# Kernel tuning notes

Measured on AMD Instinct MI355X. Metric: run time of the kernel, lower is better.

The kernel has to match this reference:

```python
import jax, jax.numpy as jnp
import numpy as np

B, NQ, NK = 4, 1024, 1536
DQ = DK = DV = 1024
DI = 4096
H = 16
EPS = 1e-5

def _ln(x, g, b):
    mu = jnp.mean(x, axis=-1, keepdims=True)
    var = jnp.mean((x - mu) ** 2, axis=-1, keepdims=True)
    return (x - mu) * jax.lax.rsqrt(var + EPS) * g + b

def setup_inputs() -> dict:
    key = jax.random.key(0)
    ks = jax.random.split(key, 20)
    s = 0.02
    inp = {
        "Q": jax.random.normal(ks[0], (B, NQ, DQ), jnp.float32),
        "K": jax.random.normal(ks[1], (B, NK, DK), jnp.float32),
        "knn_masks": jax.random.normal(ks[2], (B * H, NQ, 1024), jnp.float32),
        "mask_pos": 1024,
        "Wq": jax.random.normal(ks[3], (DQ, DV), jnp.float32) * s,
        "bq": jnp.zeros((DV,), jnp.float32),
        "Wk": jax.random.normal(ks[4], (DK, DV), jnp.float32) * s,
        "bk": jnp.zeros((DV,), jnp.float32),
        "Wv": jax.random.normal(ks[5], (DK, DV), jnp.float32) * s,
        "bv": jnp.zeros((DV,), jnp.float32),
        "Wo0": jax.random.normal(ks[6], (DV, DV), jnp.float32) * s,
        "bo0": jnp.zeros((DV,), jnp.float32),
        "Wo": jax.random.normal(ks[7], (DV, DI), jnp.float32) * s,
        "bo": jnp.zeros((DI,), jnp.float32),
        "Wo2": jax.random.normal(ks[8], (DI, DV), jnp.float32) * s,
        "bo2": jnp.zeros((DV,), jnp.float32),
        "g0": jnp.ones((DV,), jnp.float32),
        "beta0": jnp.zeros((DV,), jnp.float32),
        "g1": jnp.ones((DV,), jnp.float32),
        "beta1": jnp.zeros((DV,), jnp.float32),
    }
    return inp

def reference(Q, K, knn_masks, mask_pos, Wq, bq, Wk, bk, Wv, bv,
              Wo0, bo0, Wo, bo, Wo2, bo2, g0, beta0, g1, beta1):
    dh = DV // H
    q = Q @ Wq + bq                      # [B,NQ,DV]
    k = K @ Wk + bk                      # [B,NK,DV]
    v = K @ Wv + bv
    # torch cat(split(.,dh,2),0) -> head-major [H,B,N,dh]
    qh = q.reshape(B, NQ, H, dh).transpose(2, 0, 1, 3)
    kh = k[:, :mask_pos].reshape(B, mask_pos, H, dh).transpose(2, 0, 1, 3)
    vh = v[:, :mask_pos].reshape(B, mask_pos, H, dh).transpose(2, 0, 1, 3)
    logits = jnp.einsum("hbqd,hbkd->hbqk", qh, kh) / jnp.sqrt(jnp.float32(DV))
    logits = logits + knn_masks.reshape(H, B, NQ, mask_pos)
    attn = jax.nn.softmax(logits, axis=-1)
    o = jnp.einsum("hbqk,hbkd->hbqd", attn, vh)   # [H,B,NQ,dh]
    o = o.transpose(1, 2, 0, 3).reshape(B, NQ, DV)  # concat heads
    o = o @ Wo0 + bo0
    O = q + o
    O = _ln(O, g0, beta0)
    ff = jax.nn.relu(O @ Wo + bo) @ Wo2 + bo2
    O = O + ff
    O = _ln(O, g1, beta1)
    return O
```

## Files before the change

### kernel.cpp

```cpp
#include <hip/hip_runtime.h>
#include <hip/hip_bf16.h>

typedef unsigned short u16;
typedef __attribute__((ext_vector_type(4))) short bf16x4;
typedef __attribute__((ext_vector_type(8))) short bf16x8;
typedef __attribute__((ext_vector_type(4))) float f32x4;

static __device__ __forceinline__ u16 f2b(float f){
  union { float f; unsigned u; } v; v.f = f;
  unsigned r = v.u + 0x7fffu + ((v.u >> 16) & 1u);
  return (u16)(r >> 16);
}
static __device__ __forceinline__ float b2f(u16 h){
  union { unsigned u; float f; } v; v.u = ((unsigned)h) << 16; return v.f;
}
static __device__ __forceinline__ void gld_lds16(const void* g, void* l){
  __builtin_amdgcn_global_load_lds((const __attribute__((address_space(1))) void*)g,
                                   (__attribute__((address_space(3))) void*)l, 16, 0, 0);
}

__global__ __launch_bounds__(256) void cvt_qk(const float* __restrict__ Q,
                                              const float* __restrict__ K,
                                              u16* __restrict__ Qb,
                                              u16* __restrict__ Kb){
  const int row = blockIdx.x, t = threadIdx.x;
  const float* src; u16* dst;
  if (row < 4096){
    src = Q + (size_t)row * 1024; dst = Qb + (size_t)row * 1024;
  } else {
    int r = row - 4096;
    size_t ir = (size_t)r + (size_t)(r >> 10) * 512;
    src = K + ir * 1024; dst = Kb + (size_t)r * 1024;
  }
  const float4 v = *(const float4*)(src + t * 4);
  bf16x4 o;
  o[0] = (short)f2b(v.x); o[1] = (short)f2b(v.y);
  o[2] = (short)f2b(v.z); o[3] = (short)f2b(v.w);
  *(bf16x4*)(dst + t * 4) = o;
}

static __device__ __forceinline__ void transpose_body(const float* __restrict__ in,
                                                      u16* __restrict__ out, int K, int N){
  __shared__ float tile[64][65];
  const int k0 = blockIdx.y * 64, n0 = blockIdx.x * 64;
  const int t = threadIdx.x, tr = t >> 4, tc = t & 15;
#pragma unroll
  for (int i = 0; i < 4; i++){
    int r = tr + i * 16;
    float4 v = *(const float4*)(in + (size_t)(k0 + r) * N + n0 + tc * 4);
    tile[r][tc*4+0] = v.x; tile[r][tc*4+1] = v.y; tile[r][tc*4+2] = v.z; tile[r][tc*4+3] = v.w;
  }
  __syncthreads();
#pragma unroll
  for (int i = 0; i < 4; i++){
    int nr = tr + i * 16;
    bf16x4 pk;
#pragma unroll
    for (int j = 0; j < 4; j++) pk[j] = (short)f2b(tile[tc*4+j][nr]);
    *(bf16x4*)(out + (size_t)(n0 + nr) * K + k0 + tc * 4) = pk;
  }
}

__global__ __launch_bounds__(256) void transpose_cvt_k(const float* __restrict__ in,
                                                       u16* __restrict__ out, int K, int N){
  transpose_body(in, out, K, N);
}

__global__ __launch_bounds__(256) void transpose_cvt4(const float* __restrict__ i0, u16* __restrict__ o0,
                                                      const float* __restrict__ i1, u16* __restrict__ o1,
                                                      const float* __restrict__ i2, u16* __restrict__ o2,
                                                      const float* __restrict__ i3, u16* __restrict__ o3){
  const float* in; u16* out;
  switch (blockIdx.z){
    case 0: in = i0; out = o0; break;
    case 1: in = i1; out = o1; break;
    case 2: in = i2; out = o2; break;
    default: in = i3; out = o3; break;
  }
  transpose_body(in, out, 1024, 1024);
}

static __device__ __forceinline__ void gemm_mainloop(const u16* __restrict__ A,
                                                     const u16* __restrict__ Bt,
                                                     int lda, int ldb, int kbeg, int kend,
                                                     int m0, int n0,
                                                     u16* lA, u16* lB, f32x4 acc[4][4]){
  const int t = threadIdx.x, w = t >> 6, l = t & 63;
  const int wr = w >> 1, wc = w & 1;
  const int lrow = l >> 3, lc8 = l & 7;
  const int c = l & 15, g = l >> 4;
  for (int k0 = kbeg; k0 < kend; k0 += 64){
#pragma unroll
    for (int i = 0; i < 4; i++){
      int ch = w * 4 + i;
      int r  = ch * 8 + lrow;
      gld_lds16(A  + (size_t)(m0 + r) * lda + k0 + lc8 * 8, lA + ch * 512);
      gld_lds16(Bt + (size_t)(n0 + r) * ldb + k0 + lc8 * 8, lB + ch * 512);
    }
    __syncthreads();
#pragma unroll
    for (int ks = 0; ks < 2; ks++){
      bf16x8 af[4], bfr[4];
#pragma unroll
      for (int mi = 0; mi < 4; mi++){
        int row = wr * 64 + mi * 16 + c;
        af[mi] = *(const bf16x8*)((const char*)lA + row * 128 + ks * 64 + g * 16);
      }
#pragma unroll
      for (int ni = 0; ni < 4; ni++){
        int row = wc * 64 + ni * 16 + c;
        bfr[ni] = *(const bf16x8*)((const char*)lB + row * 128 + ks * 64 + g * 16);
      }
#pragma unroll
      for (int mi = 0; mi < 4; mi++)
#pragma unroll
        for (int ni = 0; ni < 4; ni++)
          acc[mi][ni] = __builtin_amdgcn_mfma_f32_16x16x32_bf16(af[mi], bfr[ni], acc[mi][ni], 0, 0, 0);
    }
    __syncthreads();
  }
}

__global__ __launch_bounds__(256) void gemm_sk2(const u16* __restrict__ A,
                                                const u16* __restrict__ Bt,
                                                float* __restrict__ pout){
  __shared__ u16 lA[128 * 64];
  __shared__ u16 lB[128 * 64];
  const int t = threadIdx.x, w = t >> 6, l = t & 63;
  const int m0 = blockIdx.y * 128, n0 = blockIdx.x * 128;
  const int wr = w >> 1, wc = w & 1;
  const int c = l & 15, g = l >> 4;
  const int kbeg = blockIdx.z * 512;

  f32x4 acc[4][4];
#pragma unroll
  for (int i = 0; i < 4; i++)
#pragma unroll
    for (int j = 0; j < 4; j++) acc[i][j] = (f32x4){0.f, 0.f, 0.f, 0.f};

  gemm_mainloop(A, Bt, 1024, 1024, kbeg, kbeg + 512, m0, n0, lA, lB, acc);

  float* po = pout + ((size_t)blockIdx.z << 22);
#pragma unroll
  for (int ni = 0; ni < 4; ni++){
    int n = n0 + wc * 64 + ni * 16 + c;
#pragma unroll
    for (int mi = 0; mi < 4; mi++){
      int row0 = m0 + wr * 64 + mi * 16 + 4 * g;
#pragma unroll
      for (int r = 0; r < 4; r++)
        po[(size_t)(row0 + r) * 1024 + n] = acc[mi][ni][r];
    }
  }
}

static __device__ __forceinline__ void loop8p(const u16* __restrict__ A,
                                              const u16* __restrict__ Bt,
                                              int lda, int ldb, int kbeg, int NT,
                                              int m0, int n0,
                                              u16 (*sA)[2][8192], u16 (*sB)[2][8192],
                                              f32x4 acc[8][4]){
  const int t = threadIdx.x, w = t >> 6, l = t & 63;
  const int wr = w >> 2, wc = w & 3;
  const int c = l & 15, g = l >> 4;
  const int sr = t >> 3, scb = (t & 7) << 4;

  auto stA = [&](int d, int h, int T){
#pragma unroll
    for (int i = 0; i < 2; i++){
      int row = i * 64 + sr;
      int Lb  = scb ^ ((row & 7) << 4);
      gld_lds16(A + (size_t)(m0 + h * 128 + row) * lda + kbeg + T * 64 + (Lb >> 1),
                (char*)&sA[d][h][0] + i * 8192 + t * 16);
    }
  };
  auto stB = [&](int d, int h, int T){
#pragma unroll
    for (int i = 0; i < 2; i++){
      int row = i * 64 + sr;
      int Lb  = scb ^ ((row & 7) << 4);
      gld_lds16(Bt + (size_t)(n0 + h * 128 + row) * ldb + kbeg + T * 64 + (Lb >> 1),
                (char*)&sB[d][h][0] + i * 8192 + t * 16);
    }
  };

  stB(0, 0, 0); stB(0, 1, 0); stA(0, 0, 0); stA(0, 1, 0);
  stB(1, 0, 1); stB(1, 1, 1);

  bf16x8 bfr[4][2];
  for (int T = 0; T < NT; ++T){
    const int d = T & 1;
    const char* pa = (const char*)&sA[d][wr][0];
    const char* pb = (const char*)&sB[d][wc >> 1][0];
#pragma unroll
    for (int q = 0; q < 4; ++q){
      if (q == 0){
        if (T + 1 < NT) asm volatile("s_waitcnt vmcnt(4)" ::: "memory");
        else            asm volatile("s_waitcnt vmcnt(0)" ::: "memory");
        asm volatile("" ::: "memory");
        __builtin_amdgcn_s_barrier();
        asm volatile("" ::: "memory");
#pragma unroll
        for (int nf = 0; nf < 4; ++nf){
          int lr = (wc & 1) * 64 + nf * 16 + c;
#pragma unroll
          for (int ks = 0; ks < 2; ++ks)
            bfr[nf][ks] = *(const bf16x8*)(pb + lr * 128 + ((ks * 64 + g * 16) ^ ((lr & 7) << 4)));
        }
      }
      bf16x8 af[2][2];
#pragma unroll
      for (int mi = 0; mi < 2; ++mi){
        int lr = (q * 2 + mi) * 16 + c;
#pragma unroll
        for (int ks = 0; ks < 2; ++ks)
          af[mi][ks] = *(const bf16x8*)(pa + lr * 128 + ((ks * 64 + g * 16) ^ ((lr & 7) << 4)));
      }
      if      (q == 0){ if (T + 1 < NT) stA(d ^ 1, 0, T + 1); }
      else if (q == 1){ if (T + 1 < NT) stA(d ^ 1, 1, T + 1); }
      else if (q == 2){ if (T + 2 < NT) stB(d, 0, T + 2); }
      else            { if (T + 2 < NT) stB(d, 1, T + 2); }
      __builtin_amdgcn_s_setprio(1);
#pragma unroll
      for (int mi = 0; mi < 2; ++mi)
#pragma unroll
        for (int nf = 0; nf < 4; ++nf)
#pragma unroll
          for (int ks = 0; ks < 2; ++ks)
            acc[q * 2 + mi][nf] =
              __builtin_amdgcn_mfma_f32_16x16x32_bf16(af[mi][ks], bfr[nf][ks], acc[q * 2 + mi][nf], 0, 0, 0);
      __builtin_amdgcn_s_setprio(0);
      asm volatile("" ::: "memory");
      __builtin_amdgcn_s_barrier();
      asm volatile("" ::: "memory");
    }
  }
}

template<int EPI>
__global__ __launch_bounds__(512, 2) void gemm8p(const u16* __restrict__ A,
                                                 const u16* __restrict__ Bt,
                                                 const float* __restrict__ bias,
                                                 void* __restrict__ outp,
                                                 int lda, int ldb, int ldout,
                                                 int ksz, int NT){
  __shared__ u16 sA[2][2][8192];
  __shared__ u16 sB[2][2][8192];
  const int t = threadIdx.x, w = t >> 6, l = t & 63;
  const int wr = w >> 2, wc = w & 3;
  const int c = l & 15, g = l >> 4;
  const int m0 = blockIdx.y * 256, n0 = blockIdx.x * 256;

  f32x4 acc[8][4];
#pragma unroll
  for (int i = 0; i < 8; i++)
#pragma unroll
    for (int j = 0; j < 4; j++) acc[i][j] = (f32x4){0.f, 0.f, 0.f, 0.f};

  loop8p(A, Bt, lda, ldb, blockIdx.z * ksz, NT, m0, n0, sA, sB, acc);

  if (EPI == 0){
    u16* out = (u16*)outp;
#pragma unroll
    for (int nf = 0; nf < 4; ++nf){
      int n = n0 + wc * 64 + nf * 16 + c;
      float bv = bias[n];
#pragma unroll
      for (int mf = 0; mf < 8; ++mf){
        int row0 = m0 + wr * 128 + mf * 16 + 4 * g;
#pragma unroll
        for (int r = 0; r < 4; ++r)
          out[(size_t)(row0 + r) * ldout + n] = f2b(fmaxf(acc[mf][nf][r] + bv, 0.f));
      }
    }
  } else {
    float* po = (float*)outp + ((size_t)blockIdx.z << 22);
#pragma unroll
    for (int nf = 0; nf < 4; ++nf){
      int n = n0 + wc * 64 + nf * 16 + c;
#pragma unroll
      for (int mf = 0; mf < 8; ++mf){
        int row0 = m0 + wr * 128 + mf * 16 + 4 * g;
#pragma unroll
        for (int r = 0; r < 4; ++r)
          po[(size_t)(row0 + r) * 1024 + n] = acc[mf][nf][r];
      }
    }
  }
}

__global__ __launch_bounds__(512, 2) void gemm8p_qkv(const u16* __restrict__ Qb,
                                                     const u16* __restrict__ Kb,
                                                     const u16* __restrict__ Wq_t,
                                                     const u16* __restrict__ Wk_t,
                                                     const u16* __restrict__ Wv_t,
                                                     const float* __restrict__ bq,
                                                     const float* __restrict__ bk,
                                                     const float* __restrict__ bv,
                                                     u16* __restrict__ qb,
                                                     u16* __restrict__ kbf,
                                                     u16* __restrict__ vtb){
  __shared__ u16 sA[2][2][8192];
  __shared__ u16 sB[2][2][8192];
  const int bx = blockIdx.x, sel = bx >> 2;
  const u16* A    = sel ? Kb : Qb;
  const u16* Bt   = (sel == 0) ? Wq_t : (sel == 1) ? Wk_t : Wv_t;
  const float* bi = (sel == 0) ? bq   : (sel == 1) ? bk   : bv;
  const int t = threadIdx.x, w = t >> 6, l = t & 63;
  const int wr = w >> 2, wc = w & 3;
  const int c = l & 15, g = l >> 4;
  const int m0 = blockIdx.y * 256, n0 = (bx & 3) * 256;

  f32x4 acc[8][4];
#pragma unroll
  for (int i = 0; i < 8; i++)
#pragma unroll
    for (int j = 0; j < 4; j++) acc[i][j] = (f32x4){0.f, 0.f, 0.f, 0.f};

  loop8p(A, Bt, 1024, 1024, 0, 16, m0, n0, sA, sB, acc);

#pragma unroll
  for (int nf = 0; nf < 4; ++nf){
    int n = n0 + wc * 64 + nf * 16 + c;
    float bv_ = bi[n];
#pragma unroll
    for (int mf = 0; mf < 8; ++mf){
      int row0 = m0 + wr * 128 + mf * 16 + 4 * g;
      if (sel == 2){
        bf16x4 pk;
#pragma unroll
        for (int r = 0; r < 4; ++r) pk[r] = (short)f2b(acc[mf][nf][r] + bv_);
        int bb = row0 >> 10, key = row0 & 1023;
        *(bf16x4*)(vtb + ((size_t)bb << 20) + (size_t)n * 1024 + key) = pk;
      } else {
        u16* out = sel ? kbf : qb;
#pragma unroll
        for (int r = 0; r < 4; ++r)
          out[(size_t)(row0 + r) * 1024 + n] = f2b(acc[mf][nf][r] + bv_);
      }
    }
  }
}

__global__ __launch_bounds__(256) void comb_ln0(const float* __restrict__ pp,
                                                const float* __restrict__ bias,
                                                const u16* __restrict__ res,
                                                const float* __restrict__ gw,
                                                const float* __restrict__ bw,
                                                u16* __restrict__ out){
  const int row = blockIdx.x, t = threadIdx.x, w = t >> 6, l = t & 63;
  const size_t i4 = (size_t)row * 1024 + t * 4;
  f32x4 a = *(const f32x4*)(pp + i4);
  f32x4 b = *(const f32x4*)(pp + (1ull << 22) + i4);
  bf16x4 rv = *(const bf16x4*)(res + i4);
  float xs[4], s = 0.f, sq = 0.f;
#pragma unroll
  for (int j = 0; j < 4; j++){
    xs[j] = a[j] + b[j] + bias[t * 4 + j] + b2f((u16)rv[j]);
    s += xs[j]; sq += xs[j] * xs[j];
  }
#pragma unroll
  for (int o = 32; o; o >>= 1){ s += __shfl_xor(s, o); sq += __shfl_xor(sq, o); }
  __shared__ float rs[4], rq[4];
  if (l == 0){ rs[w] = s; rq[w] = sq; }
  __syncthreads();
  s  = rs[0] + rs[1] + rs[2] + rs[3];
  sq = rq[0] + rq[1] + rq[2] + rq[3];
  const float mu   = s * (1.f / 1024.f);
  const float var  = sq * (1.f / 1024.f) - mu * mu;
  const float rstd = rsqrtf(var + 1e-5f);
  bf16x4 o;
#pragma unroll
  for (int j = 0; j < 4; j++) o[j] = (short)f2b((xs[j]-mu)*rstd*gw[t*4+j] + bw[t*4+j]);
  *(bf16x4*)(out + i4) = o;
}

__global__ __launch_bounds__(256) void comb_ln1(const float* __restrict__ pp,
                                                const float* __restrict__ bias,
                                                const u16* __restrict__ res,
                                                const float* __restrict__ gw,
                                                const float* __restrict__ bw,
                                                float* __restrict__ out){
  const int row = blockIdx.x, t = threadIdx.x, w = t >> 6, l = t & 63;
  const size_t i4 = (size_t)row * 1024 + t * 4;
  f32x4 a = *(const f32x4*)(pp + i4);
#pragma unroll
  for (int z = 1; z < 4; z++){
    f32x4 p = *(const f32x4*)(pp + ((size_t)z << 22) + i4);
    a[0] += p[0]; a[1] += p[1]; a[2] += p[2]; a[3] += p[3];
  }
  bf16x4 rv = *(const bf16x4*)(res + i4);
  float xs[4], s = 0.f, sq = 0.f;
#pragma unroll
  for (int j = 0; j < 4; j++){
    xs[j] = a[j] + bias[t * 4 + j] + b2f((u16)rv[j]);
    s += xs[j]; sq += xs[j] * xs[j];
  }
#pragma unroll
  for (int o = 32; o; o >>= 1){ s += __shfl_xor(s, o); sq += __shfl_xor(sq, o); }
  __shared__ float rs[4], rq[4];
  if (l == 0){ rs[w] = s; rq[w] = sq; }
  __syncthreads();
  s  = rs[0] + rs[1] + rs[2] + rs[3];
  sq = rq[0] + rq[1] + rq[2] + rq[3];
  const float mu   = s * (1.f / 1024.f);
  const float var  = sq * (1.f / 1024.f) - mu * mu;
  const float rstd = rsqrtf(var + 1e-5f);
  float4 o4;
  o4.x = (xs[0]-mu)*rstd*gw[t*4+0] + bw[t*4+0];
  o4.y = (xs[1]-mu)*rstd*gw[t*4+1] + bw[t*4+1];
  o4.z = (xs[2]-mu)*rstd*gw[t*4+2] + bw[t*4+2];
  o4.w = (xs[3]-mu)*rstd*gw[t*4+3] + bw[t*4+3];
  *((float4*)out + (size_t)row * 256 + t) = o4;
}

__global__ __launch_bounds__(256, 4) void attn_k(const u16* __restrict__ qb,
                                                 const u16* __restrict__ kb,
                                                 const u16* __restrict__ vt,
                                                 const float* __restrict__ mask,
                                                 u16* __restrict__ ob){
  __shared__ u16 sK[2][4096];
  __shared__ u16 sV[2][4096];

  const int t = threadIdx.x, w = t >> 6, l = t & 63;
  const int c = l & 15, g = l >> 4;
  const int q0 = blockIdx.x * 64, h = blockIdx.y, b = blockIdx.z;
  const int qrow = q0 + w * 16 + c;
  const size_t qoff = ((size_t)(b * 1024 + qrow)) * 1024 + h * 64;
  const bf16x8 bq0 = *(const bf16x8*)(qb + qoff + g * 8);
  const bf16x8 bq1 = *(const bf16x8*)(qb + qoff + 32 + g * 8);
  const u16* kbase = kb + ((size_t)b * 1024) * 1024 + h * 64;
  const u16* vbase = vt + ((size_t)b << 20) + (size_t)(h * 64) * 1024;
  const float* mbase = mask + ((size_t)(h * 4 + b) * 1024 + qrow) * 1024;

  const int lr3 = l >> 3, lc3 = l & 7;
  const int ch0 = w * 2;

  auto stage = [&](int buf, int kv){
#pragma unroll
    for (int i = 0; i < 2; i++){
      int ch  = ch0 + i;
      int row = ch * 8 + lr3;
      int L   = (lc3 * 16) ^ ((row & 7) << 4);
      gld_lds16(kbase + (size_t)(kv + row) * 1024 + (L >> 1), &sK[buf][ch * 512]);
      gld_lds16(vbase + (size_t)row * 1024 + kv + (L >> 1),   &sV[buf][ch * 512]);
    }
  };

  float m = -INFINITY, lsum = 0.f;
  f32x4 acc[4];
#pragma unroll
  for (int f = 0; f < 4; f++) acc[f] = (f32x4){0.f, 0.f, 0.f, 0.f};

  stage(0, 0);
  asm volatile("" ::: "memory");
  f32x4 mc[4], mn[4];
#pragma unroll
  for (int nf = 0; nf < 4; nf++) mc[nf] = *(const f32x4*)(mbase + nf * 16 + g * 4);

  const int sw = (c & 7) << 4;
  int cur = 0;
  for (int it = 0; it < 16; ++it){
    const int kv = it * 64;
    asm volatile("s_waitcnt vmcnt(4)" ::: "memory");
    __builtin_amdgcn_s_barrier();
    asm volatile("" ::: "memory");

    if (it < 15){
      stage(cur ^ 1, kv + 64);
      asm volatile("" ::: "memory");
#pragma unroll
      for (int nf = 0; nf < 4; nf++)
        mn[nf] = *(const f32x4*)(mbase + kv + 64 + nf * 16 + g * 4);
    }

    const char* kt = (const char*)sK[cur];
    f32x4 st[4];
#pragma unroll
    for (int nf = 0; nf < 4; nf++){
      const char* kr = kt + (nf * 16 + c) * 128;
      bf16x8 ak0 = *(const bf16x8*)(kr + ((g * 16) ^ sw));
      bf16x8 ak1 = *(const bf16x8*)(kr + ((64 + g * 16) ^ sw));
      f32x4 z = (f32x4){0.f, 0.f, 0.f, 0.f};
      z = __builtin_amdgcn_mfma_f32_16x16x32_bf16(ak0, bq0, z, 0, 0, 0);
      z = __builtin_amdgcn_mfma_f32_16x16x32_bf16(ak1, bq1, z, 0, 0, 0);
      st[nf] = z;
    }

    float tmax = -INFINITY;
#pragma unroll
    for (int nf = 0; nf < 4; nf++)
#pragma unroll
      for (int r = 0; r < 4; r++){
        float v = st[nf][r] * 0.03125f + mc[nf][r];
        st[nf][r] = v; tmax = fmaxf(tmax, v);
      }
    tmax = fmaxf(tmax, __shfl_xor(tmax, 16));
    tmax = fmaxf(tmax, __shfl_xor(tmax, 32));
    float mnew  = fmaxf(m, tmax);
    float alpha = __expf(m - mnew);
    float rsum = 0.f;
    bf16x4 pb[4];
#pragma unroll
    for (int nf = 0; nf < 4; nf++)
#pragma unroll
      for (int r = 0; r < 4; r++){
        float p = __expf(st[nf][r] - mnew);
        rsum += p;
        pb[nf][r] = (short)f2b(p);
      }
    rsum += __shfl_xor(rsum, 16); rsum += __shfl_xor(rsum, 32);
    lsum = lsum * alpha + rsum; m = mnew;
#pragma unroll
    for (int f = 0; f < 4; f++){
      acc[f][0] *= alpha; acc[f][1] *= alpha; acc[f][2] *= alpha; acc[f][3] *= alpha;
    }

    const char* vtc = (const char*)sV[cur];
#pragma unroll
    for (int f = 0; f < 4; f++){
      const char* vr = vtc + (f * 16 + c) * 128;
#pragma unroll
      for (int nf = 0; nf < 4; nf++){
        bf16x4 av = *(const bf16x4*)(vr + ((nf * 32 + g * 8) ^ sw));
        acc[f] = __builtin_amdgcn_mfma_f32_16x16x16bf16_1k(av, pb[nf], acc[f], 0, 0, 0);
      }
    }

    if (it < 15){
#pragma unroll
      for (int nf = 0; nf < 4; nf++) mc[nf] = mn[nf];
    }
    cur ^= 1;
  }

  const float inv = 1.f / lsum;
#pragma unroll
  for (int f = 0; f < 4; f++){
    bf16x4 pk;
#pragma unroll
    for (int r = 0; r < 4; r++) pk[r] = (short)f2b(acc[f][r] * inv);
    *(bf16x4*)(ob + qoff + f * 16 + g * 4) = pk;
  }
}

extern "C" void kernel_launch(void* const* d_in, const int* in_sizes, int n_in,
                              void* d_out, int out_size, void* d_ws, size_t ws_size,
                              hipStream_t stream){
  const float* Q    = (const float*)d_in[0];
  const float* K    = (const float*)d_in[1];
  const float* mask = (const float*)d_in[2];
  const float* Wq   = (const float*)d_in[4];  const float* bq  = (const float*)d_in[5];
  const float* Wk   = (const float*)d_in[6];  const float* bk  = (const float*)d_in[7];
  const float* Wv   = (const float*)d_in[8];  const float* bv  = (const float*)d_in[9];
  const float* Wo0  = (const float*)d_in[10]; const float* bo0 = (const float*)d_in[11];
  const float* Wo   = (const float*)d_in[12]; const float* bo  = (const float*)d_in[13];
  const float* Wo2  = (const float*)d_in[14]; const float* bo2 = (const float*)d_in[15];
  const float* g0   = (const float*)d_in[16]; const float* be0 = (const float*)d_in[17];
  const float* g1   = (const float*)d_in[18]; const float* be1 = (const float*)d_in[19];

  uint8_t* W = (uint8_t*)d_ws;
  const size_t MB = 1024ull * 1024ull;
  u16* Wq_t  = (u16*)(W + 0);
  u16* Wk_t  = (u16*)(W + 2  * MB);
  u16* Wv_t  = (u16*)(W + 4  * MB);
  u16* Wo0_t = (u16*)(W + 6  * MB);
  u16* Wo_t  = (u16*)(W + 8  * MB);
  u16* Wo2_t = (u16*)(W + 16 * MB);
  u16* Qb    = (u16*)(W + 24 * MB);
  u16* Kb    = (u16*)(W + 32 * MB);
  u16* qb    = (u16*)(W + 40 * MB);
  u16* kbf   = (u16*)(W + 48 * MB);
  u16* vtb   = (u16*)(W + 56 * MB);
  u16* ob    = (u16*)(W + 24 * MB);
  u16* x1b   = (u16*)(W + 64 * MB);
  u16* hb    = (u16*)(W + 32 * MB);
  float* pp  = (float*)(W + 72 * MB);

  cvt_qk<<<8192, 256, 0, stream>>>(Q, K, Qb, Kb);
  transpose_cvt4<<<dim3(16, 16, 4), 256, 0, stream>>>(Wq, Wq_t, Wk, Wk_t, Wv, Wv_t, Wo0, Wo0_t);
  transpose_cvt_k<<<dim3(64, 16), 256, 0, stream>>>(Wo,  Wo_t,  1024, 4096);
  transpose_cvt_k<<<dim3(16, 64), 256, 0, stream>>>(Wo2, Wo2_t, 4096, 1024);

  gemm8p_qkv<<<dim3(12, 16), 512, 0, stream>>>(Qb, Kb, Wq_t, Wk_t, Wv_t,
                                               bq, bk, bv, qb, kbf, vtb);

  attn_k<<<dim3(16, 16, 4), 256, 0, stream>>>(qb, kbf, vtb, mask, ob);

  gemm_sk2<<<dim3(8, 32, 2), 256, 0, stream>>>(ob, Wo0_t, pp);
  comb_ln0<<<4096, 256, 0, stream>>>(pp, bo0, qb, g0, be0, x1b);

  gemm8p<0><<<dim3(16, 16), 512, 0, stream>>>(x1b, Wo_t, bo, hb, 1024, 1024, 4096, 0, 16);
  gemm8p<1><<<dim3(4, 16, 4), 512, 0, stream>>>(hb, Wo2_t, nullptr, pp, 4096, 4096, 1024, 1024, 16);
  comb_ln1<<<4096, 256, 0, stream>>>(pp, bo2, x1b, g1, be1, (float*)d_out);
}
```

Measured before the change: 306.6 us.

## Merge prep kernels into one launch and unroll attention loop with mask prefetch

The four weight/input conversion kernels are merged into a single prep launch that dispatches on block index. This removes three launch gaps and lets the small transposes overlap the Q/K cast. The attention loop is manually unrolled by two with fixed LDS buffer indices, and the mask is prefetched two tiles ahead into ping-pong register sets. The PV MFMA block is also bracketed with s_setprio. These raise register pressure in attn_k and add a divergent branch structure in prep.

```diff
diff --git a/kernel.cpp b/kernel.cpp
--- a/kernel.cpp
+++ b/kernel.cpp
@@ -19,31 +19,49 @@
                                    (__attribute__((address_space(3))) void*)l, 16, 0, 0);
 }
 
-__global__ __launch_bounds__(256) void cvt_qk(const float* __restrict__ Q,
-                                              const float* __restrict__ K,
-                                              u16* __restrict__ Qb,
-                                              u16* __restrict__ Kb){
-  const int row = blockIdx.x, t = threadIdx.x;
-  const float* src; u16* dst;
-  if (row < 4096){
-    src = Q + (size_t)row * 1024; dst = Qb + (size_t)row * 1024;
+__global__ __launch_bounds__(256) void prep(const float* __restrict__ Q,
+                                            const float* __restrict__ K,
+                                            u16* __restrict__ Qb, u16* __restrict__ Kb,
+                                            const float* __restrict__ Wq, u16* __restrict__ Wq_t,
+                                            const float* __restrict__ Wk, u16* __restrict__ Wk_t,
+                                            const float* __restrict__ Wv, u16* __restrict__ Wv_t,
+                                            const float* __restrict__ Wo0, u16* __restrict__ Wo0_t,
+                                            const float* __restrict__ Wo, u16* __restrict__ Wo_t,
+                                            const float* __restrict__ Wo2, u16* __restrict__ Wo2_t){
+  __shared__ float tile[64][65];
+  const int id = blockIdx.x, t = threadIdx.x;
+  if (id < 8192){
+    const float* src; u16* dst;
+    if (id < 4096){
+      src = Q + (size_t)id * 1024; dst = Qb + (size_t)id * 1024;
+    } else {
+      int r = id - 4096;
+      size_t ir = (size_t)r + (size_t)(r >> 10) * 512;
+      src = K + ir * 1024; dst = Kb + (size_t)r * 1024;
+    }
+    const float4 v = *(const float4*)(src + t * 4);
+    bf16x4 o;
+    o[0] = (short)f2b(v.x); o[1] = (short)f2b(v.y);
+    o[2] = (short)f2b(v.z); o[3] = (short)f2b(v.w);
+    *(bf16x4*)(dst + t * 4) = o;
+    return;
+  }
+  int wid = id - 8192;
+  const float* in; u16* out; int Kd, N, bx, by;
+  if (wid < 1024){
+    int sel = wid >> 8, local = wid & 255;
+    bx = local & 15; by = local >> 4; Kd = 1024; N = 1024;
+    in  = (sel == 0) ? Wq   : (sel == 1) ? Wk   : (sel == 2) ? Wv   : Wo0;
+    out = (sel == 0) ? Wq_t : (sel == 1) ? Wk_t : (sel == 2) ? Wv_t : Wo0_t;
+  } else if (wid < 2048){
+    int local = wid - 1024; bx = local & 63; by = local >> 6; Kd = 1024; N = 4096;
+    in = Wo; out = Wo_t;
   } else {
-    int r = row - 4096;
-    size_t ir = (size_t)r + (size_t)(r >> 10) * 512;
-    src = K + ir * 1024; dst = Kb + (size_t)r * 1024;
-  }
-  const float4 v = *(const float4*)(src + t * 4);
-  bf16x4 o;
-  o[0] = (short)f2b(v.x); o[1] = (short)f2b(v.y);
-  o[2] = (short)f2b(v.z); o[3] = (short)f2b(v.w);
-  *(bf16x4*)(dst + t * 4) = o;
-}
-
-static __device__ __forceinline__ void transpose_body(const float* __restrict__ in,
-                                                      u16* __restrict__ out, int K, int N){
-  __shared__ float tile[64][65];
-  const int k0 = blockIdx.y * 64, n0 = blockIdx.x * 64;
-  const int t = threadIdx.x, tr = t >> 4, tc = t & 15;
+    int local = wid - 2048; bx = local & 15; by = local >> 4; Kd = 4096; N = 1024;
+    in = Wo2; out = Wo2_t;
+  }
+  const int k0 = by * 64, n0 = bx * 64;
+  const int tr = t >> 4, tc = t & 15;
 #pragma unroll
   for (int i = 0; i < 4; i++){
     int r = tr + i * 16;
@@ -57,27 +75,8 @@
     bf16x4 pk;
 #pragma unroll
     for (int j = 0; j < 4; j++) pk[j] = (short)f2b(tile[tc*4+j][nr]);
-    *(bf16x4*)(out + (size_t)(n0 + nr) * K + k0 + tc * 4) = pk;
-  }
-}
-
-__global__ __launch_bounds__(256) void transpose_cvt_k(const float* __restrict__ in,
-                                                       u16* __restrict__ out, int K, int N){
-  transpose_body(in, out, K, N);
-}
-
-__global__ __launch_bounds__(256) void transpose_cvt4(const float* __restrict__ i0, u16* __restrict__ o0,
-                                                      const float* __restrict__ i1, u16* __restrict__ o1,
-                                                      const float* __restrict__ i2, u16* __restrict__ o2,
-                                                      const float* __restrict__ i3, u16* __restrict__ o3){
-  const float* in; u16* out;
-  switch (blockIdx.z){
-    case 0: in = i0; out = o0; break;
-    case 1: in = i1; out = o1; break;
-    case 2: in = i2; out = o2; break;
-    default: in = i3; out = o3; break;
-  }
-  transpose_body(in, out, 1024, 1024);
+    *(bf16x4*)(out + (size_t)(n0 + nr) * Kd + k0 + tc * 4) = pk;
+  }
 }
 
 static __device__ __forceinline__ void gemm_mainloop(const u16* __restrict__ A,
@@ -414,6 +413,73 @@
   *((float4*)out + (size_t)row * 256 + t) = o4;
 }
 
+#define ATTN_STEP(IT, CUR, MC) do{                                              \
+  if ((IT) < 15) asm volatile("s_waitcnt vmcnt(4)" ::: "memory");               \
+  else           asm volatile("s_waitcnt vmcnt(0)" ::: "memory");               \
+  __builtin_amdgcn_s_barrier();                                                 \
+  asm volatile("" ::: "memory");                                                \
+  if ((IT) < 15) stage((CUR) ^ 1, ((IT) + 1) * 64);                             \
+  asm volatile("" ::: "memory");                                                \
+  const char* kt = (const char*)sK[(CUR)];                                      \
+  f32x4 st[4];                                                                  \
+  _Pragma("unroll")                                                             \
+  for (int nf = 0; nf < 4; nf++){                                               \
+    const char* kr = kt + (nf * 16 + c) * 128;                                  \
+    bf16x8 ak0 = *(const bf16x8*)(kr + ((g * 16) ^ sw));                        \
+    bf16x8 ak1 = *(const bf16x8*)(kr + ((64 + g * 16) ^ sw));                   \
+    f32x4 z = (f32x4){0.f, 0.f, 0.f, 0.f};                                      \
+    z = __builtin_amdgcn_mfma_f32_16x16x32_bf16(ak0, bq0, z, 0, 0, 0);          \
+    z = __builtin_amdgcn_mfma_f32_16x16x32_bf16(ak1, bq1, z, 0, 0, 0);          \
+    st[nf] = z;                                                                 \
+  }                                                                             \
+  float tmax = -INFINITY;                                                       \
+  _Pragma("unroll")                                                             \
+  for (int nf = 0; nf < 4; nf++)                                                \
+    _Pragma("unroll")                                                           \
+    for (int r = 0; r < 4; r++){                                                \
+      float v = st[nf][r] * 0.03125f + MC[nf][r];                               \
+      st[nf][r] = v; tmax = fmaxf(tmax, v);                                     \
+    }                                                                           \
+  if ((IT) < 14){                                                               \
+    _Pragma("unroll")                                                           \
+    for (int nf = 0; nf < 4; nf++)                                              \
+      MC[nf] = *(const f32x4*)(mbase + ((IT) + 2) * 64 + nf * 16 + g * 4);      \
+  }                                                                             \
+  tmax = fmaxf(tmax, __shfl_xor(tmax, 16));                                     \
+  tmax = fmaxf(tmax, __shfl_xor(tmax, 32));                                     \
+  float mnew  = fmaxf(m, tmax);                                                 \
+  float alpha = __expf(m - mnew);                                               \
+  float rsum = 0.f;                                                             \
+  bf16x4 pb[4];                                                                 \
+  _Pragma("unroll")                                                             \
+  for (int nf = 0; nf < 4; nf++)                                                \
+    _Pragma("unroll")                                                           \
+    for (int r = 0; r < 4; r++){                                                \
+      float p = __expf(st[nf][r] - mnew);                                       \
+      rsum += p;                                                                \
+      pb[nf][r] = (short)f2b(p);                                                \
+    }                                                                           \
+  rsum += __shfl_xor(rsum, 16); rsum += __shfl_xor(rsum, 32);                   \
+  lsum = lsum * alpha + rsum; m = mnew;                                         \
+  _Pragma("unroll")                                                             \
+  for (int f = 0; f < 4; f++){                                                  \
+    acc[f][0] *= alpha; acc[f][1] *= alpha;                                     \
+    acc[f][2] *= alpha; acc[f][3] *= alpha;                                     \
+  }                                                                             \
+  const char* vtc = (const char*)sV[(CUR)];                                     \
+  __builtin_amdgcn_s_setprio(1);                                                \
+  _Pragma("unroll")                                                             \
+  for (int f = 0; f < 4; f++){                                                  \
+    const char* vr = vtc + (f * 16 + c) * 128;                                  \
+    _Pragma("unroll")                                                           \
+    for (int nf = 0; nf < 4; nf++){                                             \
+      bf16x4 av = *(const bf16x4*)(vr + ((nf * 32 + g * 8) ^ sw));              \
+      acc[f] = __builtin_amdgcn_mfma_f32_16x16x16bf16_1k(av, pb[nf], acc[f], 0, 0, 0); \
+    }                                                                           \
+  }                                                                             \
+  __builtin_amdgcn_s_setprio(0);                                                \
+}while(0)
+
 __global__ __launch_bounds__(256, 4) void attn_k(const u16* __restrict__ qb,
                                                  const u16* __restrict__ kb,
                                                  const u16* __restrict__ vt,
@@ -454,84 +520,17 @@
 
   stage(0, 0);
   asm volatile("" ::: "memory");
-  f32x4 mc[4], mn[4];
-#pragma unroll
-  for (int nf = 0; nf < 4; nf++) mc[nf] = *(const f32x4*)(mbase + nf * 16 + g * 4);
+  f32x4 mA[4], mB[4];
+#pragma unroll
+  for (int nf = 0; nf < 4; nf++) mA[nf] = *(const f32x4*)(mbase + nf * 16 + g * 4);
+  asm volatile("" ::: "memory");
+#pragma unroll
+  for (int nf = 0; nf < 4; nf++) mB[nf] = *(const f32x4*)(mbase + 64 + nf * 16 + g * 4);
 
   const int sw = (c & 7) << 4;
-  int cur = 0;
-  for (int it = 0; it < 16; ++it){
-    const int kv = it * 64;
-    asm volatile("s_waitcnt vmcnt(4)" ::: "memory");
-    __builtin_amdgcn_s_barrier();
-    asm volatile("" ::: "memory");
-
-    if (it < 15){
-      stage(cur ^ 1, kv + 64);
-      asm volatile("" ::: "memory");
-#pragma unroll
-      for (int nf = 0; nf < 4; nf++)
-        mn[nf] = *(const f32x4*)(mbase + kv + 64 + nf * 16 + g * 4);
-    }
-
-    const char* kt = (const char*)sK[cur];
-    f32x4 st[4];
-#pragma unroll
-    for (int nf = 0; nf < 4; nf++){
-      const char* kr = kt + (nf * 16 + c) * 128;
-      bf16x8 ak0 = *(const bf16x8*)(kr + ((g * 16) ^ sw));
-      bf16x8 ak1 = *(const bf16x8*)(kr + ((64 + g * 16) ^ sw));
-      f32x4 z = (f32x4){0.f, 0.f, 0.f, 0.f};
-      z = __builtin_amdgcn_mfma_f32_16x16x32_bf16(ak0, bq0, z, 0, 0, 0);
-      z = __builtin_amdgcn_mfma_f32_16x16x32_bf16(ak1, bq1, z, 0, 0, 0);
-      st[nf] = z;
-    }
-
-    float tmax = -INFINITY;
-#pragma unroll
-    for (int nf = 0; nf < 4; nf++)
-#pragma unroll
-      for (int r = 0; r < 4; r++){
-        float v = st[nf][r] * 0.03125f + mc[nf][r];
-        st[nf][r] = v; tmax = fmaxf(tmax, v);
-      }
-    tmax = fmaxf(tmax, __shfl_xor(tmax, 16));
-    tmax = fmaxf(tmax, __shfl_xor(tmax, 32));
-    float mnew  = fmaxf(m, tmax);
-    float alpha = __expf(m - mnew);
-    float rsum = 0.f;
-    bf16x4 pb[4];
-#pragma unroll
-    for (int nf = 0; nf < 4; nf++)
-#pragma unroll
-      for (int r = 0; r < 4; r++){
-        float p = __expf(st[nf][r] - mnew);
-        rsum += p;
-        pb[nf][r] = (short)f2b(p);
-      }
-    rsum += __shfl_xor(rsum, 16); rsum += __shfl_xor(rsum, 32);
-    lsum = lsum * alpha + rsum; m = mnew;
-#pragma unroll
-    for (int f = 0; f < 4; f++){
-      acc[f][0] *= alpha; acc[f][1] *= alpha; acc[f][2] *= alpha; acc[f][3] *= alpha;
-    }
-
-    const char* vtc = (const char*)sV[cur];
-#pragma unroll
-    for (int f = 0; f < 4; f++){
-      const char* vr = vtc + (f * 16 + c) * 128;
-#pragma unroll
-      for (int nf = 0; nf < 4; nf++){
-        bf16x4 av = *(const bf16x4*)(vr + ((nf * 32 + g * 8) ^ sw));
-        acc[f] = __builtin_amdgcn_mfma_f32_16x16x16bf16_1k(av, pb[nf], acc[f], 0, 0, 0);
-      }
-    }
-
-    if (it < 15){
-#pragma unroll
-      for (int nf = 0; nf < 4; nf++) mc[nf] = mn[nf];
-    }
-    cur ^= 1;
+  for (int ii = 0; ii < 8; ++ii){
+    ATTN_STEP(2 * ii,     0, mA);
+    ATTN_STEP(2 * ii + 1, 1, mB);
   }
 
   const float inv = 1.f / lsum;
@@ -577,10 +576,8 @@
   u16* hb    = (u16*)(W + 32 * MB);
   float* pp  = (float*)(W + 72 * MB);
 
-  cvt_qk<<<8192, 256, 0, stream>>>(Q, K, Qb, Kb);
-  transpose_cvt4<<<dim3(16, 16, 4), 256, 0, stream>>>(Wq, Wq_t, Wk, Wk_t, Wv, Wv_t, Wo0, Wo0_t);
-  transpose_cvt_k<<<dim3(64, 16), 256, 0, stream>>>(Wo,  Wo_t,  1024, 4096);
-  transpose_cvt_k<<<dim3(16, 64), 256, 0, stream>>>(Wo2, Wo2_t, 4096, 1024);
+  prep<<<11264, 256, 0, stream>>>(Q, K, Qb, Kb, Wq, Wq_t, Wk, Wk_t, Wv, Wv_t,
+                                  Wo0, Wo0_t, Wo, Wo_t, Wo2, Wo2_t);
 
   gemm8p_qkv<<<dim3(12, 16), 512, 0, stream>>>(Qb, Kb, Wq_t, Wk_t, Wv_t,
                                                bq, bk, bv, qb, kbf, vtb);
```

Measured after the change: 302.5 us. Within noise of the previous version (-1.3%).
